# Optimization experiments

Measured on AMD Instinct MI355X. Metric: run time of the kernel, lower is better.

## Reference

```python
import math
import jax, jax.numpy as jnp
import numpy as np

VMIN, VMAX, NUM_BINS = 0.0, 1.0, 64
BIN_WIDTH = (VMAX - VMIN) / NUM_BINS
SIGMA = BIN_WIDTH * (1.0 / (2.0 * math.sqrt(2.0 * math.log(2.0))))
EPS = 1e-10


def setup_inputs() -> dict:
    key = jax.random.key(0)
    kx, ky = jax.random.split(key)
    shape = (2, 1, 96, 96, 96)
    x = jax.random.uniform(kx, shape, dtype=jnp.float32)
    y = jax.random.uniform(ky, shape, dtype=jnp.float32)
    return {"x": x, "y": y}


def _gauss_win(v, bins):
    # v: (N, P), bins: (B,) -> (N, B, P)
    d = v[:, None, :] - bins[None, :, None]
    # NOTE: faithful to source: exp(.)/sqrt(2*pi) * sigma (multiplies by sigma)
    return jnp.exp(-(d * d) / (2.0 * SIGMA * SIGMA)) / math.sqrt(2.0 * math.pi) * SIGMA


def reference(x, y):
    N = x.shape[0]
    xf = x.reshape(N, -1)  # (N, P); dim=1 channel folded into P
    yf = y.reshape(N, -1)
    bins = jnp.linspace(VMIN, VMAX, NUM_BINS, dtype=x.dtype)
    win_x = _gauss_win(xf, bins)  # (N, B, P)
    win_y = _gauss_win(yf, bins)  # (N, B, P)
    hist_joint = jnp.einsum('nbp,ncp->nbc', win_x, win_y)  # (N, B, B)
    hist_norm = hist_joint.sum(axis=(1, 2)) + EPS
    p_joint = hist_joint / hist_norm[:, None, None]
    p_x = p_joint.sum(axis=2)
    p_y = p_joint.sum(axis=1)
    ent_x = -jnp.sum(p_x * jnp.log(p_x + EPS), axis=1)
    ent_y = -jnp.sum(p_y * jnp.log(p_y + EPS), axis=1)
    ent_joint = -jnp.sum(p_joint * jnp.log(p_joint + EPS), axis=(1, 2))
    # normalised=True branch
    return -jnp.mean((ent_x + ent_y) / ent_joint)
```

## Files before the change

kernel.cpp:

```cpp
#include <hip/hip_runtime.h>
#include <math.h>


#define NBINS 64
#define BK 128
#define TILE (NBINS * BK)
#define NKB 8

#define SWZ(r) ((((r) >> 3) ^ (r)) & 7)
#define CHIDX(r, c) ((r) * BK + ((((c) & 8) | (((c) ^ SWZ(r)) & 7)) << 3))

typedef _Float16 half8    __attribute__((ext_vector_type(8)));
typedef float    floatx16 __attribute__((ext_vector_type(16)));

static constexpr double kSigmaD = 0.015625 / 2.3548200450309493;
static constexpr double kAcD    = (1.0 / (63.0 * 63.0)) / (2.0 * kSigmaD * kSigmaD);
static constexpr float  kAc     = (float)kAcD;
static constexpr float  kEps    = 1e-10f;

__device__ __forceinline__ void make_w(float v, int& c, float* w) {
    c = min(max((int)(v + 0.5f), 2), 61);
    const float d = v - (float)c;
#pragma unroll
    for (int k = 0; k < 5; ++k) {
        const float dd = d - (float)(k - 2);
        w[k] = __expf(-kAc * dd * dd);
    }
}

__global__ __launch_bounds__(256, 2) void hist_gemm_kernel(
        const float* __restrict__ x, const float* __restrict__ y,
        float* __restrict__ hist, int P, int elemsPerBlock) {
    __shared__ __align__(16) _Float16 tiles[4 * TILE];

    const int t    = threadIdx.x;
    const int lane = t & 63;
    const int wave = t >> 6;
    const int m    = lane & 31;
    const int kq8  = lane >> 5;
    const int n    = blockIdx.y;
    const int col  = t & 127;
    const bool isX = (t < 128);

    {
        float* z4 = (float*)tiles;
        for (int i = t; i < 4 * TILE / 2; i += 256) z4[i] = 0.0f;
    }

    floatx16 acc[2][2];
#pragma unroll
    for (int bi = 0; bi < 2; ++bi)
#pragma unroll
        for (int bj = 0; bj < 2; ++bj) acc[bi][bj] = (floatx16){};

    const float* __restrict__ src = (isX ? x : y) + (size_t)n * P;
    const int base    = blockIdx.x * elemsPerBlock;
    const int nChunks = elemsPerBlock / BK;

    _Float16* myTile = tiles + (isX ? 0 : TILE);
    const int cc0 = col >> 3;
    const int cw  = col & 7;

    int pc[2] = {2, 2};

    {
        int ctr; float w[5];
        make_w(src[base + col] * 63.0f, ctr, w);
#pragma unroll
        for (int k = 0; k < 5; ++k) {
            const int r = ctr - 2 + k;
            myTile[CHIDX(r, cc0) + cw] = (_Float16)w[k];
        }
        pc[0] = ctr;
    }
    __syncthreads();

    for (int c = 0; c < nChunks; ++c) {
        const int b  = c & 1;
        const int nb = b ^ 1;
        const bool more = (c + 1 < nChunks);

        float v = 0.0f;
        if (more) v = src[base + (c + 1) * BK + col] * 63.0f;

        const _Float16* Axb = tiles + b * 2 * TILE;
        const _Float16* Byb = Axb + TILE;
#pragma unroll
        for (int s = 0; s < 2; ++s) {
            const int kb = wave + 4 * s;
            const int ch = 2 * kb + kq8;
            const int r0 = m, r1 = 32 + m;
            const half8 a0 = *(const half8*)&Axb[CHIDX(r0, ch)];
            const half8 a1 = *(const half8*)&Axb[CHIDX(r1, ch)];
            const half8 b0 = *(const half8*)&Byb[CHIDX(r0, ch)];
            const half8 b1 = *(const half8*)&Byb[CHIDX(r1, ch)];
            acc[0][0] = __builtin_amdgcn_mfma_f32_32x32x16_f16(a0, b0, acc[0][0], 0, 0, 0);
            acc[0][1] = __builtin_amdgcn_mfma_f32_32x32x16_f16(a0, b1, acc[0][1], 0, 0, 0);
            acc[1][0] = __builtin_amdgcn_mfma_f32_32x32x16_f16(a1, b0, acc[1][0], 0, 0, 0);
            acc[1][1] = __builtin_amdgcn_mfma_f32_32x32x16_f16(a1, b1, acc[1][1], 0, 0, 0);
        }

        if (more) {
            int ctr; float w[5];
            make_w(v, ctr, w);
            _Float16* st = myTile + nb * 2 * TILE;
            const int po = pc[nb];
#pragma unroll
            for (int k = 0; k < 5; ++k) {
                const int r = po - 2 + k;
                st[CHIDX(r, cc0) + cw] = (_Float16)0.0f;
            }
#pragma unroll
            for (int k = 0; k < 5; ++k) {
                const int r = ctr - 2 + k;
                st[CHIDX(r, cc0) + cw] = (_Float16)w[k];
            }
            pc[nb] = ctr;
        }
        __syncthreads();
    }

    float* cred = (float*)tiles;
    const int rbase = 4 * kq8;

    if (wave >= 2) {
        const int off = (wave - 2) * 4096;
#pragma unroll
        for (int bi = 0; bi < 2; ++bi)
#pragma unroll
            for (int bj = 0; bj < 2; ++bj)
#pragma unroll
                for (int r = 0; r < 16; ++r) {
                    const int row = bi * 32 + (r & 3) + 8 * (r >> 2) + rbase;
                    const int cl  = bj * 32 + m;
                    cred[off + row * NBINS + cl] = acc[bi][bj][r];
                }
    }
    __syncthreads();
    if (wave < 2) {
        const int off = wave * 4096;
#pragma unroll
        for (int bi = 0; bi < 2; ++bi)
#pragma unroll
            for (int bj = 0; bj < 2; ++bj)
#pragma unroll
                for (int r = 0; r < 16; ++r) {
                    const int row = bi * 32 + (r & 3) + 8 * (r >> 2) + rbase;
                    const int cl  = bj * 32 + m;
                    const int idx = off + row * NBINS + cl;
                    cred[idx] = acc[bi][bj][r] + cred[idx];
                }
    }
    __syncthreads();
    float* __restrict__ gh = hist + (size_t)n * NBINS * NBINS;
    for (int i = t; i < NBINS * NBINS; i += 256)
        atomicAdd(&gh[i], cred[i] + cred[4096 + i]);
}

__device__ __forceinline__ float block_sum_bcast(float v, float* sm) {
#pragma unroll
    for (int off = 32; off > 0; off >>= 1) v += __shfl_down(v, off, 64);
    __syncthreads();
    const int lane = threadIdx.x & 63;
    const int wid  = threadIdx.x >> 6;
    if (lane == 0) sm[wid] = v;
    __syncthreads();
    return sm[0] + sm[1] + sm[2] + sm[3];
}

__global__ __launch_bounds__(256) void finalize_kernel(
        const float* __restrict__ hist, float* __restrict__ out) {
    __shared__ float sm[4];
    __shared__ float sx[NBINS];
    __shared__ float sy[NBINS];

    const int n = blockIdx.x;
    const float* __restrict__ h = hist + (size_t)n * NBINS * NBINS;

    float s = 0.0f;
    for (int i = threadIdx.x; i < NBINS * NBINS; i += 256) s += h[i];
    const float S = block_sum_bcast(s, sm) + kEps;
    const float invS = 1.0f / S;

    float ej = 0.0f;
    for (int i = threadIdx.x; i < NBINS * NBINS; i += 256) {
        const float p = h[i] * invS;
        ej += p * __logf(p + kEps);
    }

    if (threadIdx.x < NBINS) {
        float px = 0.0f;
        const float* rp = &h[threadIdx.x * NBINS];
        for (int c = 0; c < NBINS; c++) px += rp[c];
        px *= invS;
        sx[threadIdx.x] = px * __logf(px + kEps);
    } else if (threadIdx.x < 2 * NBINS) {
        const int c = threadIdx.x - NBINS;
        float py = 0.0f;
        for (int b = 0; b < NBINS; b++) py += h[b * NBINS + c];
        py *= invS;
        sy[c] = py * __logf(py + kEps);
    }

    const float EJ = block_sum_bcast(ej, sm);
    const float mx = (threadIdx.x < NBINS) ? sx[threadIdx.x] : 0.0f;
    const float my = (threadIdx.x < NBINS) ? sy[threadIdx.x] : 0.0f;
    const float EX = block_sum_bcast(mx, sm);
    const float EY = block_sum_bcast(my, sm);

    if (threadIdx.x == 0) atomicAdd(out, -0.5f * ((EX + EY) / EJ));
}

extern "C" void kernel_launch(void* const* d_in, const int* in_sizes, int n_in,
                              void* d_out, int out_size, void* d_ws, size_t ws_size,
                              hipStream_t stream) {
    const float* x = (const float*)d_in[0];
    const float* y = (const float*)d_in[1];
    float* hist = (float*)d_ws;
    float* out  = (float*)d_out;

    const int N = 2;
    const int P = in_sizes[0] / N;
    const int blocksPerN = 256;
    const int elemsPerBlock = P / blocksPerN;

    hipMemsetAsync(hist, 0, (size_t)N * NBINS * NBINS * sizeof(float), stream);
    hipMemsetAsync(out, 0, sizeof(float), stream);

    dim3 grid(blocksPerN, N);
    hist_gemm_kernel<<<grid, 256, 0, stream>>>(x, y, hist, P, elemsPerBlock);

    finalize_kernel<<<2, 256, 0, stream>>>(hist, out);
}
```

Measured before the change: 108.1 us.

## Fuse entropy finalize into histogram kernel and preload all input chunks into registers

Removes the separate finalize kernel. The last block to finish, found through a global atomic counter after a threadfence, computes both samples' entropies and writes the output directly. Each thread now loads all 27 of its input values into registers up front instead of prefetching one chunk ahead, and the chunk loop is fully unrolled with a fixed chunk count. The two memsets are merged into one, and shared-memory zeroing uses float4 stores. This adds register pressure and a serial tail in one block, and it hardcodes a chunk count that must divide the problem size.

```diff
diff --git a/kernel.cpp b/kernel.cpp
--- a/kernel.cpp
+++ b/kernel.cpp
@@ -6,6 +6,7 @@
 #define BK 128
 #define TILE (NBINS * BK)
 #define NKB 8
+#define NCHUNK 27
 
 #define SWZ(r) ((((r) >> 3) ^ (r)) & 7)
 #define CHIDX(r, c) ((r) * BK + ((((c) & 8) | (((c) ^ SWZ(r)) & 7)) << 3))
@@ -28,10 +29,23 @@
     }
 }
 
+__device__ __forceinline__ float block_sum_bcast(float v, float* sm) {
+#pragma unroll
+    for (int off = 32; off > 0; off >>= 1) v += __shfl_down(v, off, 64);
+    __syncthreads();
+    const int lane = threadIdx.x & 63;
+    const int wid  = threadIdx.x >> 6;
+    if (lane == 0) sm[wid] = v;
+    __syncthreads();
+    return sm[0] + sm[1] + sm[2] + sm[3];
+}
+
 __global__ __launch_bounds__(256, 2) void hist_gemm_kernel(
         const float* __restrict__ x, const float* __restrict__ y,
-        float* __restrict__ hist, int P, int elemsPerBlock) {
+        float* __restrict__ hist, unsigned* __restrict__ counter,
+        float* __restrict__ out, int P, int totalBlocks) {
     __shared__ __align__(16) _Float16 tiles[4 * TILE];
+    __shared__ unsigned rank;
 
     const int t    = threadIdx.x;
     const int lane = t & 63;
@@ -43,8 +57,9 @@
     const bool isX = (t < 128);
 
     {
-        float* z4 = (float*)tiles;
-        for (int i = t; i < 4 * TILE / 2; i += 256) z4[i] = 0.0f;
+        float4* z = (float4*)tiles;
+#pragma unroll
+        for (int i = 0; i < 16; ++i) z[t + 256 * i] = make_float4(0.f, 0.f, 0.f, 0.f);
     }
 
     floatx16 acc[2][2];
@@ -54,34 +69,31 @@
         for (int bj = 0; bj < 2; ++bj) acc[bi][bj] = (floatx16){};
 
     const float* __restrict__ src = (isX ? x : y) + (size_t)n * P;
-    const int base    = blockIdx.x * elemsPerBlock;
-    const int nChunks = elemsPerBlock / BK;
+    const int base = blockIdx.x * (BK * NCHUNK);
+
+    float vals[NCHUNK];
+#pragma unroll
+    for (int c = 0; c < NCHUNK; ++c) vals[c] = src[base + c * BK + col];
 
     _Float16* myTile = tiles + (isX ? 0 : TILE);
     const int cc0 = col >> 3;
     const int cw  = col & 7;
 
-    int pc[2] = {2, 2};
+    int pc0 = 2, pc1 = 2;
 
     {
         int ctr; float w[5];
-        make_w(src[base + col] * 63.0f, ctr, w);
-#pragma unroll
-        for (int k = 0; k < 5; ++k) {
-            const int r = ctr - 2 + k;
-            myTile[CHIDX(r, cc0) + cw] = (_Float16)w[k];
-        }
-        pc[0] = ctr;
-    }
-    __syncthreads();
-
-    for (int c = 0; c < nChunks; ++c) {
-        const int b  = c & 1;
-        const int nb = b ^ 1;
-        const bool more = (c + 1 < nChunks);
-
-        float v = 0.0f;
-        if (more) v = src[base + (c + 1) * BK + col] * 63.0f;
+        make_w(vals[0] * 63.0f, ctr, w);
+#pragma unroll
+        for (int k = 0; k < 5; ++k)
+            myTile[CHIDX(ctr - 2 + k, cc0) + cw] = (_Float16)w[k];
+        pc0 = ctr;
+    }
+    __syncthreads();
+
+#pragma unroll
+    for (int c = 0; c < NCHUNK; ++c) {
+        const int b = c & 1;
 
         const _Float16* Axb = tiles + b * 2 * TILE;
         const _Float16* Byb = Axb + TILE;
@@ -89,33 +101,28 @@
         for (int s = 0; s < 2; ++s) {
             const int kb = wave + 4 * s;
             const int ch = 2 * kb + kq8;
-            const int r0 = m, r1 = 32 + m;
-            const half8 a0 = *(const half8*)&Axb[CHIDX(r0, ch)];
-            const half8 a1 = *(const half8*)&Axb[CHIDX(r1, ch)];
-            const half8 b0 = *(const half8*)&Byb[CHIDX(r0, ch)];
-            const half8 b1 = *(const half8*)&Byb[CHIDX(r1, ch)];
+            const half8 a0 = *(const half8*)&Axb[CHIDX(m, ch)];
+            const half8 a1 = *(const half8*)&Axb[CHIDX(32 + m, ch)];
+            const half8 b0 = *(const half8*)&Byb[CHIDX(m, ch)];
+            const half8 b1 = *(const half8*)&Byb[CHIDX(32 + m, ch)];
             acc[0][0] = __builtin_amdgcn_mfma_f32_32x32x16_f16(a0, b0, acc[0][0], 0, 0, 0);
             acc[0][1] = __builtin_amdgcn_mfma_f32_32x32x16_f16(a0, b1, acc[0][1], 0, 0, 0);
             acc[1][0] = __builtin_amdgcn_mfma_f32_32x32x16_f16(a1, b0, acc[1][0], 0, 0, 0);
             acc[1][1] = __builtin_amdgcn_mfma_f32_32x32x16_f16(a1, b1, acc[1][1], 0, 0, 0);
         }
 
-        if (more) {
+        if (c + 1 < NCHUNK) {
             int ctr; float w[5];
-            make_w(v, ctr, w);
-            _Float16* st = myTile + nb * 2 * TILE;
-            const int po = pc[nb];
-#pragma unroll
-            for (int k = 0; k < 5; ++k) {
-                const int r = po - 2 + k;
-                st[CHIDX(r, cc0) + cw] = (_Float16)0.0f;
-            }
-#pragma unroll
-            for (int k = 0; k < 5; ++k) {
-                const int r = ctr - 2 + k;
-                st[CHIDX(r, cc0) + cw] = (_Float16)w[k];
-            }
-            pc[nb] = ctr;
+            make_w(vals[c + 1] * 63.0f, ctr, w);
+            _Float16* st = myTile + (b ^ 1) * 2 * TILE;
+            const int po = (b ^ 1) ? pc1 : pc0;
+#pragma unroll
+            for (int k = 0; k < 5; ++k)
+                st[CHIDX(po - 2 + k, cc0) + cw] = (_Float16)0.0f;
+#pragma unroll
+            for (int k = 0; k < 5; ++k)
+                st[CHIDX(ctr - 2 + k, cc0) + cw] = (_Float16)w[k];
+            if (b ^ 1) pc1 = ctr; else pc0 = ctr;
         }
         __syncthreads();
     }
@@ -155,60 +162,60 @@
     float* __restrict__ gh = hist + (size_t)n * NBINS * NBINS;
     for (int i = t; i < NBINS * NBINS; i += 256)
         atomicAdd(&gh[i], cred[i] + cred[4096 + i]);
-}
-
-__device__ __forceinline__ float block_sum_bcast(float v, float* sm) {
-#pragma unroll
-    for (int off = 32; off > 0; off >>= 1) v += __shfl_down(v, off, 64);
-    __syncthreads();
-    const int lane = threadIdx.x & 63;
-    const int wid  = threadIdx.x >> 6;
-    if (lane == 0) sm[wid] = v;
-    __syncthreads();
-    return sm[0] + sm[1] + sm[2] + sm[3];
-}
-
-__global__ __launch_bounds__(256) void finalize_kernel(
-        const float* __restrict__ hist, float* __restrict__ out) {
-    __shared__ float sm[4];
-    __shared__ float sx[NBINS];
-    __shared__ float sy[NBINS];
-
-    const int n = blockIdx.x;
-    const float* __restrict__ h = hist + (size_t)n * NBINS * NBINS;
-
-    float s = 0.0f;
-    for (int i = threadIdx.x; i < NBINS * NBINS; i += 256) s += h[i];
-    const float S = block_sum_bcast(s, sm) + kEps;
-    const float invS = 1.0f / S;
-
-    float ej = 0.0f;
-    for (int i = threadIdx.x; i < NBINS * NBINS; i += 256) {
-        const float p = h[i] * invS;
-        ej += p * __logf(p + kEps);
-    }
-
-    if (threadIdx.x < NBINS) {
-        float px = 0.0f;
-        const float* rp = &h[threadIdx.x * NBINS];
-        for (int c = 0; c < NBINS; c++) px += rp[c];
-        px *= invS;
-        sx[threadIdx.x] = px * __logf(px + kEps);
-    } else if (threadIdx.x < 2 * NBINS) {
-        const int c = threadIdx.x - NBINS;
-        float py = 0.0f;
-        for (int b = 0; b < NBINS; b++) py += h[b * NBINS + c];
-        py *= invS;
-        sy[c] = py * __logf(py + kEps);
-    }
-
-    const float EJ = block_sum_bcast(ej, sm);
-    const float mx = (threadIdx.x < NBINS) ? sx[threadIdx.x] : 0.0f;
-    const float my = (threadIdx.x < NBINS) ? sy[threadIdx.x] : 0.0f;
-    const float EX = block_sum_bcast(mx, sm);
-    const float EY = block_sum_bcast(my, sm);
-
-    if (threadIdx.x == 0) atomicAdd(out, -0.5f * ((EX + EY) / EJ));
+
+    __threadfence();
+    if (t == 0) rank = atomicAdd(counter, 1u);
+    __syncthreads();
+    if (rank != (unsigned)(totalBlocks - 1)) return;
+
+    float* fs = (float*)tiles;
+    float* sm = fs;
+    float* sx = fs + 8;
+    float* sy = fs + 8 + NBINS;
+    float* hc = fs + 256;
+
+    float res = 0.0f;
+    for (int nn = 0; nn < 2; ++nn) {
+        const float* __restrict__ h = hist + (size_t)nn * NBINS * NBINS;
+        for (int i = t; i < NBINS * NBINS; i += 256)
+            hc[i] = __hip_atomic_load(&h[i], __ATOMIC_RELAXED, __HIP_MEMORY_SCOPE_AGENT);
+        __syncthreads();
+
+        float s = 0.0f;
+        for (int i = t; i < NBINS * NBINS; i += 256) s += hc[i];
+        const float S = block_sum_bcast(s, sm) + kEps;
+        const float invS = 1.0f / S;
+
+        float ej = 0.0f;
+        for (int i = t; i < NBINS * NBINS; i += 256) {
+            const float p = hc[i] * invS;
+            ej += p * __logf(p + kEps);
+        }
+
+        if (t < NBINS) {
+            float px = 0.0f;
+            const float* rp = &hc[t * NBINS];
+            for (int c = 0; c < NBINS; c++) px += rp[c];
+            px *= invS;
+            sx[t] = px * __logf(px + kEps);
+        } else if (t < 2 * NBINS) {
+            const int c = t - NBINS;
+            float py = 0.0f;
+            for (int b = 0; b < NBINS; b++) py += hc[b * NBINS + c];
+            py *= invS;
+            sy[c] = py * __logf(py + kEps);
+        }
+
+        const float EJ = block_sum_bcast(ej, sm);
+        const float mx = (t < NBINS) ? sx[t] : 0.0f;
+        const float my = (t < NBINS) ? sy[t] : 0.0f;
+        const float EX = block_sum_bcast(mx, sm);
+        const float EY = block_sum_bcast(my, sm);
+
+        res += (EX + EY) / EJ;
+        __syncthreads();
+    }
+    if (t == 0) out[0] = -0.5f * res;
 }
 
 extern "C" void kernel_launch(void* const* d_in, const int* in_sizes, int n_in,
@@ -217,18 +224,16 @@
     const float* x = (const float*)d_in[0];
     const float* y = (const float*)d_in[1];
     float* hist = (float*)d_ws;
+    unsigned* counter = (unsigned*)((char*)d_ws + 32768);
     float* out  = (float*)d_out;
 
     const int N = 2;
     const int P = in_sizes[0] / N;
-    const int blocksPerN = 256;
-    const int elemsPerBlock = P / blocksPerN;
-
-    hipMemsetAsync(hist, 0, (size_t)N * NBINS * NBINS * sizeof(float), stream);
-    hipMemsetAsync(out, 0, sizeof(float), stream);
+    const int blocksPerN = P / (BK * NCHUNK);
+    const int totalBlocks = N * blocksPerN;
+
+    hipMemsetAsync(d_ws, 0, 32768 + 64, stream);
 
     dim3 grid(blocksPerN, N);
-    hist_gemm_kernel<<<grid, 256, 0, stream>>>(x, y, hist, P, elemsPerBlock);
-
-    finalize_kernel<<<2, 256, 0, stream>>>(hist, out);
-}
+    hist_gemm_kernel<<<grid, 256, 0, stream>>>(x, y, hist, counter, out, P, totalBlocks);
+}
```

After: 126.5 us. 17.0% more time.
